# Kernel optimization log

Measured on AMD Instinct MI355X. Metric: run time of the kernel, lower is better.

Reference implementation:

```python
import jax, jax.numpy as jnp
import numpy as np

B, S, H, I, E = 2, 2048, 1024, 4096, 8


def setup_inputs() -> dict:
    key = jax.random.key(0)
    k1, k2, k3, k4 = jax.random.split(key, 4)
    hidden_states = jax.random.normal(k1, (B, S, H), dtype=jnp.float32)
    # router: nn.Linear(H, E, bias=False) -> weight (E, H)
    Wr = jax.random.normal(k2, (E, H), dtype=jnp.float32) * 0.02
    # per-expert MLP: Linear(H,I) weight (I,H); Linear(I,H) weight (H,I); stacked over E
    W1 = jax.random.normal(k3, (E, I, H), dtype=jnp.float32) * 0.02
    W2 = jax.random.normal(k4, (E, H, I), dtype=jnp.float32) * 0.02
    return {"hidden_states": hidden_states, "Wr": Wr, "W1": W1, "W2": W2}


def reference(hidden_states, Wr, W1, W2):
    b, s, h = hidden_states.shape
    n_exp = Wr.shape[0]
    x = hidden_states.reshape(-1, h)                      # (N, H)
    logits = x @ Wr.T                                     # (N, E)
    probs = jax.nn.softmax(logits, axis=-1)               # (N, E)
    # top_k with k == num_experts: sorted probs descending (one-hot mask then
    # covers every expert, so each expert sees every token; expert i's output is
    # weighted by the i-th largest prob, exactly as the torch code does).
    top_probs, _ = jax.lax.top_k(probs, n_exp)            # (N, E)
    hmid = jnp.einsum('nh,eih->nei', x, W1)               # (N, E, I)
    hmid = jax.nn.gelu(hmid, approximate=False)           # exact erf GELU (torch nn.GELU default)
    yexp = jnp.einsum('nei,ehi->neh', hmid, W2)           # (N, E, H)
    out = jnp.einsum('neh,ne->nh', yexp, top_probs)       # weighted combine
    return out.reshape(b, s, h)
```

## Files before the change

kernel.cpp:

```cpp
#include <hip/hip_runtime.h>
#include <hip/hip_bf16.h>

#define NTOK 4096
#define HD   1024
#define ID   4096
#define NE   8

typedef float  floatx4 __attribute__((ext_vector_type(4)));
typedef __bf16 bf16x8  __attribute__((ext_vector_type(8)));
typedef unsigned short u16;

__device__ __forceinline__ u16 f2bf(float f) {
    union { float f; unsigned int i; } c; c.f = f;
    return (u16)((c.i + 0x7fffu + ((c.i >> 16) & 1u)) >> 16);
}

__device__ __forceinline__ void async_copy16(u16* lds, const u16* g) {
    __builtin_amdgcn_global_load_lds(
        (const __attribute__((address_space(1))) void*)g,
        (__attribute__((address_space(3))) void*)lds, 16, 0, 0);
}

__device__ __forceinline__ float gelu_fast(float v) {
    const float u = v * (0.7978845608f + 0.0356774081f * v * v);
    const float t = 1.f - 2.f / (__expf(2.f * u) + 1.f);
    return 0.5f * v * (1.f + t);
}

#define FENCE()   asm volatile("" ::: "memory")
#define BAR()     do { FENCE(); __builtin_amdgcn_s_barrier(); FENCE(); } while (0)
#define WAITALL() asm volatile("s_waitcnt vmcnt(0) lgkmcnt(0)" ::: "memory")

__global__ __launch_bounds__(256) void convert_kernel(
    const float* __restrict__ src, u16* __restrict__ dst)
{
    const size_t i = ((size_t)blockIdx.x * 256 + threadIdx.x) * 8;
    const float4 a = *(const float4*)(src + i);
    const float4 b = *(const float4*)(src + i + 4);
    ushort4 o0, o1;
    o0.x = f2bf(a.x); o0.y = f2bf(a.y); o0.z = f2bf(a.z); o0.w = f2bf(a.w);
    o1.x = f2bf(b.x); o1.y = f2bf(b.y); o1.z = f2bf(b.z); o1.w = f2bf(b.w);
    *(ushort4*)(dst + i)     = o0;
    *(ushort4*)(dst + i + 4) = o1;
}

__global__ __launch_bounds__(256) void convert2_kernel(
    const float* __restrict__ s1, u16* __restrict__ d1,
    const float* __restrict__ s2, u16* __restrict__ d2, int half)
{
    const int b = blockIdx.x;
    const float* src = (b < half) ? s1 : s2;
    u16*         dst = (b < half) ? d1 : d2;
    const int    bb  = (b < half) ? b : b - half;
    const size_t i = ((size_t)bb * 256 + threadIdx.x) * 8;
    const float4 a = *(const float4*)(src + i);
    const float4 c = *(const float4*)(src + i + 4);
    ushort4 o0, o1;
    o0.x = f2bf(a.x); o0.y = f2bf(a.y); o0.z = f2bf(a.z); o0.w = f2bf(a.w);
    o1.x = f2bf(c.x); o1.y = f2bf(c.y); o1.z = f2bf(c.z); o1.w = f2bf(c.w);
    *(ushort4*)(dst + i)     = o0;
    *(ushort4*)(dst + i + 4) = o1;
}

__global__ __launch_bounds__(256) void router_kernel(
    const float* __restrict__ x, const float* __restrict__ Wr,
    float* __restrict__ wbuf)
{
    const int n    = blockIdx.x * 4 + (threadIdx.x >> 6);
    const int lane = threadIdx.x & 63;
    const float* xr = x + (size_t)n * HD;
    float acc[NE];
#pragma unroll
    for (int e = 0; e < NE; ++e) acc[e] = 0.f;
    for (int h = lane; h < HD; h += 64) {
        const float xv = xr[h];
#pragma unroll
        for (int e = 0; e < NE; ++e) acc[e] += xv * Wr[e * HD + h];
    }
#pragma unroll
    for (int e = 0; e < NE; ++e) {
        float v = acc[e];
#pragma unroll
        for (int off = 32; off > 0; off >>= 1) v += __shfl_xor(v, off, 64);
        acc[e] = v;
    }
    float mx = acc[0];
#pragma unroll
    for (int e = 1; e < NE; ++e) mx = fmaxf(mx, acc[e]);
    float s = 0.f;
#pragma unroll
    for (int e = 0; e < NE; ++e) { acc[e] = __expf(acc[e] - mx); s += acc[e]; }
    const float inv = 1.f / s;
#pragma unroll
    for (int e = 0; e < NE; ++e) acc[e] *= inv;
#pragma unroll
    for (int i = 0; i < NE - 1; ++i)
#pragma unroll
        for (int j = 0; j < NE - 1 - i; ++j) {
            const float a = acc[j], b = acc[j + 1];
            acc[j] = fmaxf(a, b); acc[j + 1] = fminf(a, b);
        }
    if (lane < NE) wbuf[lane * NTOK + n] = acc[lane];
}

__device__ __forceinline__ void gemm256_tile(
    const u16* __restrict__ A, const u16* __restrict__ B,
    int ldA, int ldB, int K, int rowBase, int colBase,
    u16* As0, u16* As1, u16* Bs0, u16* Bs1,
    floatx4 acc[8][4])
{
    const int t    = threadIdx.x;
    const int w    = t >> 6, lane = t & 63;
    const int wm   = w & 1, wn = w >> 1;
    const int quad = lane >> 4, l15 = lane & 15;

    const int srow   = (w << 4) + (lane >> 2);
    const int schunk = ((lane & 3) ^ ((lane >> 3) & 3)) << 3;
    const u16* gA = A + (size_t)(rowBase + srow) * ldA + schunk;
    const u16* gB = B + (size_t)(colBase + srow) * ldB + schunk;
    const size_t hA = (size_t)128 * ldA, hB = (size_t)128 * ldB;
    u16* lA0 = As0 + w * 512;
    u16* lA1 = As1 + w * 512;
    u16* lB0 = Bs0 + w * 512;
    u16* lB1 = Bs1 + w * 512;

    const int sw = (l15 >> 1) & 3;
    int aoff[8], boff[4];
#pragma unroll
    for (int mi = 0; mi < 8; ++mi)
        aoff[mi] = (wm * 128 + mi * 16 + l15) * 32 + ((quad ^ sw) << 3);
#pragma unroll
    for (int ni = 0; ni < 4; ++ni)
        boff[ni] = (wn * 64 + ni * 16 + l15) * 32 + ((quad ^ sw) << 3);

#define STAGE2(lA, lB, kt) do { const int _ko = (kt) << 5;          \
        async_copy16(lA,        gA + _ko);                          \
        async_copy16(lA + 4096, gA + _ko + hA);                     \
        async_copy16(lB,        gB + _ko);                          \
        async_copy16(lB + 4096, gB + _ko + hB); } while (0)

#define RD(P, o) (*(const bf16x8*)((P) + (o)))
#define MM4(AF, m) do {                                                     \
        __builtin_amdgcn_s_setprio(1);                                      \
        acc[m][0] = __builtin_amdgcn_mfma_f32_16x16x32_bf16(AF, b0, acc[m][0], 0, 0, 0); \
        acc[m][1] = __builtin_amdgcn_mfma_f32_16x16x32_bf16(AF, b1, acc[m][1], 0, 0, 0); \
        acc[m][2] = __builtin_amdgcn_mfma_f32_16x16x32_bf16(AF, b2, acc[m][2], 0, 0, 0); \
        acc[m][3] = __builtin_amdgcn_mfma_f32_16x16x32_bf16(AF, b3, acc[m][3], 0, 0, 0); \
        __builtin_amdgcn_s_setprio(0); } while (0)

    const int nkt = K >> 5;
    STAGE2(lA0, lB0, 0);

#pragma unroll 1
    for (int kt = 0; kt < nkt; ++kt) {
        const u16* Ab = (kt & 1) ? As1 : As0;
        const u16* Bb = (kt & 1) ? Bs1 : Bs0;
        u16* sA = (kt & 1) ? lA0 : lA1;
        u16* sB = (kt & 1) ? lB0 : lB1;
        WAITALL();
        BAR();
        if (kt + 1 < nkt) STAGE2(sA, sB, kt + 1);
        bf16x8 b0 = RD(Bb, boff[0]), b1 = RD(Bb, boff[1]);
        bf16x8 b2 = RD(Bb, boff[2]), b3 = RD(Bb, boff[3]);
        bf16x8 a0 = RD(Ab, aoff[0]), a1 = RD(Ab, aoff[1]);
        bf16x8 a2 = RD(Ab, aoff[2]);  MM4(a0, 0);
        bf16x8 a3 = RD(Ab, aoff[3]);  MM4(a1, 1);
        bf16x8 a4 = RD(Ab, aoff[4]);  MM4(a2, 2);
        bf16x8 a5 = RD(Ab, aoff[5]);  MM4(a3, 3);
        bf16x8 a6 = RD(Ab, aoff[6]);  MM4(a4, 4);
        bf16x8 a7 = RD(Ab, aoff[7]);  MM4(a5, 5);
        MM4(a6, 6);
        MM4(a7, 7);
    }
#undef STAGE2
#undef RD
#undef MM4
}

__global__ __launch_bounds__(512, 2) void gemm1_kernel(
    const u16* __restrict__ X, const u16* __restrict__ W1b,
    const float* __restrict__ wbuf, u16* __restrict__ hmid)
{
    __shared__ __align__(16) u16 As[2][8192];
    __shared__ __align__(16) u16 Bs[2][8192];
    floatx4 acc[8][4] = {};
    const int bid = blockIdx.x;
    const int x   = bid & 7;
    const int j   = bid >> 3;
    const int sub = j >> 7;
    const int nt  = x * 16 + sub * 8 + (j & 7);
    const int mt  = (j >> 3) & 15;
    const int rowBase = mt * 256, colBase = nt * 256;
    const int e  = colBase >> 12;
    const int ic0 = colBase & (ID - 1);

    gemm256_tile(X, W1b, HD, HD, HD, rowBase, colBase,
                 As[0], As[1], Bs[0], Bs[1], acc);

    u16* hm = hmid + (size_t)e * NTOK * ID;
    const int t = threadIdx.x, w = t >> 6, lane = t & 63;
    const int wm = w & 1, wn = w >> 1, quad = lane >> 4, l15 = lane & 15;
#pragma unroll
    for (int mi = 0; mi < 8; ++mi)
#pragma unroll
        for (int r = 0; r < 4; ++r) {
            const int row = rowBase + wm * 128 + mi * 16 + quad * 4 + r;
            const float wv = wbuf[e * NTOK + row];
#pragma unroll
            for (int ni = 0; ni < 4; ++ni) {
                const int ic = ic0 + wn * 64 + ni * 16 + l15;
                hm[(size_t)row * ID + ic] =
                    f2bf(gelu_fast(acc[mi][ni][r]) * wv);
            }
        }
}

__global__ __launch_bounds__(512, 2) void gemm2_kernel(
    const u16* __restrict__ hmid, const u16* __restrict__ W2b,
    float* __restrict__ acclo, float* __restrict__ acchi)
{
    __shared__ __align__(16) u16 As[2][8192];
    __shared__ __align__(16) u16 Bs[2][8192];
    floatx4 acc[8][4] = {};
    const int bid = blockIdx.x;
    const int swz = (bid & 7) * 64 + (bid >> 3);
    const int z = swz >> 6, mt = (swz >> 2) & 15, nt = swz & 3;
    const int rowBase = mt * 256, colBase = nt * 256;

    gemm256_tile(hmid + (size_t)z * NTOK * ID, W2b + (size_t)z * HD * ID,
                 ID, ID, ID, rowBase, colBase,
                 As[0], As[1], Bs[0], Bs[1], acc);

    const size_t NH = (size_t)NTOK * HD;
    float* accs = (z < 4) ? (acclo + (size_t)z * NH)
                          : (acchi + (size_t)(z - 4) * NH);
    const int t = threadIdx.x, w = t >> 6, lane = t & 63;
    const int wm = w & 1, wn = w >> 1, quad = lane >> 4, l15 = lane & 15;
#pragma unroll
    for (int mi = 0; mi < 8; ++mi)
#pragma unroll
        for (int r = 0; r < 4; ++r) {
            const int row = rowBase + wm * 128 + mi * 16 + quad * 4 + r;
#pragma unroll
            for (int ni = 0; ni < 4; ++ni) {
                const int col = colBase + wn * 64 + ni * 16 + l15;
                accs[(size_t)row * HD + col] = acc[mi][ni][r];
            }
        }
}

__global__ __launch_bounds__(256) void finalize_kernel(
    const float* __restrict__ acclo, const float* __restrict__ acchi,
    float* __restrict__ out)
{
    const size_t NH = (size_t)NTOK * HD;
    const size_t i = ((size_t)blockIdx.x * 256 + threadIdx.x) * 4;
    float4 o = *(const float4*)(acclo + i);
#pragma unroll
    for (int z = 1; z < 4; ++z) {
        const float4 a = *(const float4*)(acclo + (size_t)z * NH + i);
        o.x += a.x; o.y += a.y; o.z += a.z; o.w += a.w;
    }
#pragma unroll
    for (int z = 0; z < 4; ++z) {
        const float4 a = *(const float4*)(acchi + (size_t)z * NH + i);
        o.x += a.x; o.y += a.y; o.z += a.z; o.w += a.w;
    }
    *(float4*)(out + i) = o;
}

extern "C" void kernel_launch(void* const* d_in, const int* in_sizes, int n_in,
                              void* d_out, int out_size, void* d_ws, size_t ws_size,
                              hipStream_t stream) {
    const float* x  = (const float*)d_in[0];
    const float* Wr = (const float*)d_in[1];
    const float* W1 = (const float*)d_in[2];
    const float* W2 = (const float*)d_in[3];
    float* out = (float*)d_out;

    const size_t MB = 1024 * 1024;
    char* ws = (char*)d_ws;
    float* wbuf   = (float*)ws;
    u16*   Xb     = (u16*)(ws + 131072);
    u16*   W1b    = (u16*)(ws + 131072 + 8 * MB);
    u16*   W2b    = (u16*)(ws + 131072 + 72 * MB);
    u16*   hmid   = (u16*)(ws + 131072 + 136 * MB);
    float* acclo  = (float*)ws;
    float* acchi  = (float*)(ws + 131072 + 392 * MB);
    if (ws_size < 131072 + 456 * MB) return;

    convert_kernel<<<dim3((NTOK * HD) / 2048), 256, 0, stream>>>(x, Xb);
    convert2_kernel<<<dim3(2 * (NE * ID * HD) / 2048), 256, 0, stream>>>(
        W1, W1b, W2, W2b, (NE * ID * HD) / 2048);
    router_kernel<<<dim3(NTOK / 4), 256, 0, stream>>>(x, Wr, wbuf);

    gemm1_kernel<<<dim3(NE * ID / 256 * (NTOK / 256)), 512, 0, stream>>>(
        Xb, W1b, wbuf, hmid);
    gemm2_kernel<<<dim3((NTOK / 256) * (HD / 256) * 8), 512, 0, stream>>>(
        hmid, W2b, acclo, acchi);
    finalize_kernel<<<dim3(NTOK * HD / 1024), 256, 0, stream>>>(
        acclo, acchi, out);
}
```

Before: 1.084 ms.

## Double the GEMM K-tile to 64 with an 8-way XOR-swizzled LDS layout

The shared 256x256 GEMM tile now stages 64 K-elements per iteration instead of 32, using an 8-chunk XOR swizzle for the async global-to-LDS copies and the fragment reads. Each iteration runs two 32-wide MFMA half-steps, which halves the number of barriers and wait points per K. LDS per block doubles to 128 KB, so the two-blocks-per-CU occupancy set in launch bounds may no longer be reachable. All A fragments are also loaded up front, raising register pressure.

Result: faster. 1.009 ms (-6.9%).

```diff
diff --git a/kernel.cpp b/kernel.cpp
--- a/kernel.cpp
+++ b/kernel.cpp
@@ -27,9 +27,10 @@
     return 0.5f * v * (1.f + t);
 }
 
-#define FENCE()   asm volatile("" ::: "memory")
-#define BAR()     do { FENCE(); __builtin_amdgcn_s_barrier(); FENCE(); } while (0)
-#define WAITALL() asm volatile("s_waitcnt vmcnt(0) lgkmcnt(0)" ::: "memory")
+#define FENCE()  asm volatile("" ::: "memory")
+#define BAR()    do { FENCE(); __builtin_amdgcn_s_barrier(); FENCE(); } while (0)
+#define WAITV0() asm volatile("s_waitcnt vmcnt(0)" ::: "memory")
+#define WAITL0() asm volatile("s_waitcnt lgkmcnt(0)" ::: "memory")
 
 __global__ __launch_bounds__(256) void convert_kernel(
     const float* __restrict__ src, u16* __restrict__ dst)
@@ -114,30 +115,34 @@
     const int wm   = w & 1, wn = w >> 1;
     const int quad = lane >> 4, l15 = lane & 15;
 
-    const int srow   = (w << 4) + (lane >> 2);
-    const int schunk = ((lane & 3) ^ ((lane >> 3) & 3)) << 3;
-    const u16* gA = A + (size_t)(rowBase + srow) * ldA + schunk;
-    const u16* gB = B + (size_t)(colBase + srow) * ldB + schunk;
-    const size_t hA = (size_t)128 * ldA, hB = (size_t)128 * ldB;
-    u16* lA0 = As0 + w * 512;
-    u16* lA1 = As1 + w * 512;
-    u16* lB0 = Bs0 + w * 512;
-    u16* lB1 = Bs1 + w * 512;
-
-    const int sw = (l15 >> 1) & 3;
+    const int srow = w * 32 + (lane >> 3);
+    const int ce   = ((lane & 7) ^ ((lane >> 4) & 7)) << 3;
+    const int co   = ((lane & 7) ^ ((4 + (lane >> 4)) & 7)) << 3;
+    const u16* gAe = A + (size_t)(rowBase + srow) * ldA + ce;
+    const u16* gAo = A + (size_t)(rowBase + srow + 8) * ldA + co;
+    const u16* gBe = B + (size_t)(colBase + srow) * ldB + ce;
+    const u16* gBo = B + (size_t)(colBase + srow + 8) * ldB + co;
+    const size_t r16A = (size_t)16 * ldA, r16B = (size_t)16 * ldB;
+    const int wb = w * 2048;
+
+    const int s7 = (l15 >> 1) & 7;
     int aoff[8], boff[4];
 #pragma unroll
     for (int mi = 0; mi < 8; ++mi)
-        aoff[mi] = (wm * 128 + mi * 16 + l15) * 32 + ((quad ^ sw) << 3);
+        aoff[mi] = (wm * 128 + mi * 16 + l15) * 64 + ((quad ^ s7) << 3);
 #pragma unroll
     for (int ni = 0; ni < 4; ++ni)
-        boff[ni] = (wn * 64 + ni * 16 + l15) * 32 + ((quad ^ sw) << 3);
-
-#define STAGE2(lA, lB, kt) do { const int _ko = (kt) << 5;          \
-        async_copy16(lA,        gA + _ko);                          \
-        async_copy16(lA + 4096, gA + _ko + hA);                     \
-        async_copy16(lB,        gB + _ko);                          \
-        async_copy16(lB + 4096, gB + _ko + hB); } while (0)
+        boff[ni] = (wn * 64 + ni * 16 + l15) * 64 + ((quad ^ s7) << 3);
+
+#define STAGE8(SA, SB, ko) do {                                     \
+        async_copy16((SA) + wb,        gAe + (ko));                 \
+        async_copy16((SA) + wb + 512,  gAo + (ko));                 \
+        async_copy16((SA) + wb + 1024, gAe + (ko) + r16A);          \
+        async_copy16((SA) + wb + 1536, gAo + (ko) + r16A);          \
+        async_copy16((SB) + wb,        gBe + (ko));                 \
+        async_copy16((SB) + wb + 512,  gBo + (ko));                 \
+        async_copy16((SB) + wb + 1024, gBe + (ko) + r16B);          \
+        async_copy16((SB) + wb + 1536, gBo + (ko) + r16B); } while (0)
 
 #define RD(P, o) (*(const bf16x8*)((P) + (o)))
 #define MM4(AF, m) do {                                                     \
@@ -148,31 +153,40 @@
         acc[m][3] = __builtin_amdgcn_mfma_f32_16x16x32_bf16(AF, b3, acc[m][3], 0, 0, 0); \
         __builtin_amdgcn_s_setprio(0); } while (0)
 
-    const int nkt = K >> 5;
-    STAGE2(lA0, lB0, 0);
+    const int nkt = K >> 6;
+    STAGE8(As0, Bs0, 0);
 
 #pragma unroll 1
     for (int kt = 0; kt < nkt; ++kt) {
         const u16* Ab = (kt & 1) ? As1 : As0;
         const u16* Bb = (kt & 1) ? Bs1 : Bs0;
-        u16* sA = (kt & 1) ? lA0 : lA1;
-        u16* sB = (kt & 1) ? lB0 : lB1;
-        WAITALL();
+        u16* SA = (kt & 1) ? As0 : As1;
+        u16* SB = (kt & 1) ? Bs0 : Bs1;
+        WAITV0(); WAITL0();
         BAR();
-        if (kt + 1 < nkt) STAGE2(sA, sB, kt + 1);
-        bf16x8 b0 = RD(Bb, boff[0]), b1 = RD(Bb, boff[1]);
-        bf16x8 b2 = RD(Bb, boff[2]), b3 = RD(Bb, boff[3]);
-        bf16x8 a0 = RD(Ab, aoff[0]), a1 = RD(Ab, aoff[1]);
-        bf16x8 a2 = RD(Ab, aoff[2]);  MM4(a0, 0);
-        bf16x8 a3 = RD(Ab, aoff[3]);  MM4(a1, 1);
-        bf16x8 a4 = RD(Ab, aoff[4]);  MM4(a2, 2);
-        bf16x8 a5 = RD(Ab, aoff[5]);  MM4(a3, 3);
-        bf16x8 a6 = RD(Ab, aoff[6]);  MM4(a4, 4);
-        bf16x8 a7 = RD(Ab, aoff[7]);  MM4(a5, 5);
-        MM4(a6, 6);
-        MM4(a7, 7);
-    }
-#undef STAGE2
+        if (kt + 1 < nkt) STAGE8(SA, SB, (kt + 1) << 6);
+        {
+            bf16x8 b0 = RD(Bb, boff[0]), b1 = RD(Bb, boff[1]);
+            bf16x8 b2 = RD(Bb, boff[2]), b3 = RD(Bb, boff[3]);
+            bf16x8 a0 = RD(Ab, aoff[0]), a1 = RD(Ab, aoff[1]);
+            bf16x8 a2 = RD(Ab, aoff[2]), a3 = RD(Ab, aoff[3]);
+            bf16x8 a4 = RD(Ab, aoff[4]), a5 = RD(Ab, aoff[5]);
+            bf16x8 a6 = RD(Ab, aoff[6]), a7 = RD(Ab, aoff[7]);
+            MM4(a0, 0); MM4(a1, 1); MM4(a2, 2); MM4(a3, 3);
+            MM4(a4, 4); MM4(a5, 5); MM4(a6, 6); MM4(a7, 7);
+        }
+        {
+            bf16x8 b0 = RD(Bb, boff[0] ^ 32), b1 = RD(Bb, boff[1] ^ 32);
+            bf16x8 b2 = RD(Bb, boff[2] ^ 32), b3 = RD(Bb, boff[3] ^ 32);
+            bf16x8 a0 = RD(Ab, aoff[0] ^ 32), a1 = RD(Ab, aoff[1] ^ 32);
+            bf16x8 a2 = RD(Ab, aoff[2] ^ 32), a3 = RD(Ab, aoff[3] ^ 32);
+            bf16x8 a4 = RD(Ab, aoff[4] ^ 32), a5 = RD(Ab, aoff[5] ^ 32);
+            bf16x8 a6 = RD(Ab, aoff[6] ^ 32), a7 = RD(Ab, aoff[7] ^ 32);
+            MM4(a0, 0); MM4(a1, 1); MM4(a2, 2); MM4(a3, 3);
+            MM4(a4, 4); MM4(a5, 5); MM4(a6, 6); MM4(a7, 7);
+        }
+    }
+#undef STAGE8
 #undef RD
 #undef MM4
 }
@@ -181,8 +195,8 @@
     const u16* __restrict__ X, const u16* __restrict__ W1b,
     const float* __restrict__ wbuf, u16* __restrict__ hmid)
 {
-    __shared__ __align__(16) u16 As[2][8192];
-    __shared__ __align__(16) u16 Bs[2][8192];
+    __shared__ __align__(16) u16 As[2][16384];
+    __shared__ __align__(16) u16 Bs[2][16384];
     floatx4 acc[8][4] = {};
     const int bid = blockIdx.x;
     const int x   = bid & 7;
@@ -219,8 +233,8 @@
     const u16* __restrict__ hmid, const u16* __restrict__ W2b,
     float* __restrict__ acclo, float* __restrict__ acchi)
 {
-    __shared__ __align__(16) u16 As[2][8192];
-    __shared__ __align__(16) u16 Bs[2][8192];
+    __shared__ __align__(16) u16 As[2][16384];
+    __shared__ __align__(16) u16 Bs[2][16384];
     floatx4 acc[8][4] = {};
     const int bid = blockIdx.x;
     const int swz = (bid & 7) * 64 + (bid >> 3);
```
